# Kernel optimization log

Hardware: AMD Instinct MI355X
Metric: run time of the kernel (lower is better)

## Reference

```python
import jax, jax.numpy as jnp
import numpy as np

K = 10  # hardcoded in the module
F = 3 + 3 * K + 3 * K + K + 3  # 76-dim per-point feature


def setup_inputs() -> dict:
    key = jax.random.key(0)
    k0, k1, k2, k3, k4 = jax.random.split(key, 5)
    B, N = 4, 8192
    input_cloud = jax.random.normal(k0, (B, N, 3), dtype=jnp.float32)
    # Single shared MLP (76 -> 64 -> 3); the original instantiates a fresh
    # randomly-initialized MLP per point, which a fused kernel replaces with
    # shared weights.
    W1 = jax.random.normal(k1, (F, 64), dtype=jnp.float32) * 0.1
    b1 = jax.random.normal(k2, (64,), dtype=jnp.float32) * 0.01
    W2 = jax.random.normal(k3, (64, 3), dtype=jnp.float32) * 0.1
    b2 = jax.random.normal(k4, (3,), dtype=jnp.float32) * 0.01
    return {"input_cloud": input_cloud, "W1": W1, "b1": b1, "W2": W2, "b2": b2}


def _knn_indices(cloud):
    # squared pairwise distances (same ordering as cdist), topk smallest
    sq = jnp.sum(cloud * cloud, axis=-1)  # [B,N]
    d2 = sq[:, :, None] + sq[:, None, :] - 2.0 * jnp.einsum("bnd,bmd->bnm", cloud, cloud)
    _, idx = jax.lax.top_k(-d2, K + 1)  # [B,N,K+1], smallest first (self at 0)
    return idx[:, :, 1:]  # drop self -> [B,N,K]


def reference(input_cloud, W1, b1, W2, b2):
    B, N, _ = input_cloud.shape
    knn_idx = _knn_indices(input_cloud)  # [B,N,K] int32

    # gather neighbors: [B,N,K,3]
    neighbors = jnp.take_along_axis(input_cloud[:, None, :, :],
                                    knn_idx[:, :, :, None], axis=2)
    center = input_cloud  # [B,N,3]
    rel = neighbors - center[:, :, None, :]           # [B,N,K,3]
    dists = jnp.sqrt(jnp.sum(rel * rel, axis=-1))     # [B,N,K]

    # per-point 3x3 covariance of the K neighbors (unbiased, like torch.cov)
    mean = jnp.mean(neighbors, axis=2, keepdims=True)  # [B,N,1,3]
    cen = neighbors - mean
    cov = jnp.einsum("bnki,bnkj->bnij", cen, cen) / (K - 1)  # [B,N,3,3]

    eig = jnp.linalg.eigvalsh(cov)          # ascending [B,N,3]
    l1, l2, l3 = eig[..., 2], eig[..., 1], eig[..., 0]  # descending order
    linearity = (l1 - l2) / l1
    planarity = (l2 - l3) / l1
    scattering = l3 / l1
    geom = jnp.stack([linearity, planarity, scattering], axis=-1)  # [B,N,3]

    feats = jnp.concatenate(
        [center,
         neighbors.reshape(B, N, 3 * K),
         rel.reshape(B, N, 3 * K),
         dists,
         geom], axis=-1)  # [B,N,76]

    h = jax.nn.relu(jnp.einsum("bnf,fh->bnh", feats, W1) + b1)
    out = jax.nn.relu(jnp.einsum("bnh,ho->bno", h, W2) + b2)  # [B,N,3]
    return out
```

## Files before the change

### kernel.cpp

```cpp
#include <hip/hip_runtime.h>
#include <math.h>

#define KNN    10
#define NPTS   8192
#define HID    64
#define NF     76
#define Q      16
#define CAP    64
#define F32_INF __uint_as_float(0x7F800000u)

typedef float v2f __attribute__((ext_vector_type(2)));

__device__ __forceinline__ float rl(float v, int lane) {
    return __int_as_float(__builtin_amdgcn_readlane(__float_as_int(v), lane));
}

__global__ __launch_bounds__(256) void soa_kernel(const float* __restrict__ cloud,
                                                  float* __restrict__ soa) {
    const int i = blockIdx.x * 256 + threadIdx.x;
    const float x = cloud[i * 3 + 0];
    const float y = cloud[i * 3 + 1];
    const float z = cloud[i * 3 + 2];
    soa[i]             = x;
    soa[4 * NPTS + i]  = y;
    soa[8 * NPTS + i]  = z;
}

__global__ __launch_bounds__(512) void knn_kernel(const float* __restrict__ soa,
                                                  unsigned short* __restrict__ knn_idx) {
    __shared__ unsigned long long coll[CAP][33];
    __shared__ float pk[8][Q][17];
    __shared__ float tau_s[32];
    __shared__ int   cnt[32];

    const int t    = threadIdx.x;
    const int w    = t >> 6;
    const int lane = t & 63;
    const int g    = w >> 2;
    const int h    = w & 3;
    const int bx   = blockIdx.x;
    const int b    = bx >> 8;
    const int n_base = (bx & 255) * 32 + g * Q;
    const int lq_base = g * Q;
    const int cb0 = h * (NPTS / 4);

    const float* __restrict__ xs = soa + (size_t)b * NPTS;
    const float* __restrict__ ys = xs + 4 * NPTS;
    const float* __restrict__ zs = xs + 8 * NPTS;

    if (t < 32) cnt[t] = 0;

    v2f qx_p[8], qy_p[8], qz_p[8];
    {
        const int ql = n_base + (lane & 15);
        const float lx = xs[ql];
        const float ly = ys[ql];
        const float lz = zs[ql];
#pragma unroll
        for (int j = 0; j < 8; ++j) {
            qx_p[j] = (v2f){ rl(lx, 2 * j), rl(lx, 2 * j + 1) };
            qy_p[j] = (v2f){ rl(ly, 2 * j), rl(ly, 2 * j + 1) };
            qz_p[j] = (v2f){ rl(lz, 2 * j), rl(lz, 2 * j + 1) };
        }
    }

    v2f vmin2[8];
#pragma unroll
    for (int j = 0; j < 8; ++j) vmin2[j] = (v2f){ F32_INF, F32_INF };

    {
        float cx0 = xs[cb0 + lane];
        float cy0 = ys[cb0 + lane];
        float cz0 = zs[cb0 + lane];
        for (int ti = 0; ti < NPTS / 4 / 64; ++ti) {
            const int c1 = cb0 + (((ti + 1) & 31) * 64) + lane;
            const float nx0 = xs[c1];
            const float ny0 = ys[c1];
            const float nz0 = zs[c1];
            const float aw  = fmaf(cz0, cz0, fmaf(cy0, cy0, cx0 * cx0));
            const v2f aw2  = (v2f){ aw, aw };
            const v2f a2x2 = (v2f){ -2.0f * cx0, -2.0f * cx0 };
            const v2f a2y2 = (v2f){ -2.0f * cy0, -2.0f * cy0 };
            const v2f a2z2 = (v2f){ -2.0f * cz0, -2.0f * cz0 };
#pragma unroll
            for (int j = 0; j < 8; ++j) {
                const v2f v = __builtin_elementwise_fma(a2x2, qx_p[j],
                              __builtin_elementwise_fma(a2y2, qy_p[j],
                              __builtin_elementwise_fma(a2z2, qz_p[j], aw2)));
                vmin2[j] = __builtin_elementwise_min(vmin2[j], v);
            }
            cx0 = nx0; cy0 = ny0; cz0 = nz0;
        }
    }

#pragma unroll
    for (int qq = 0; qq < Q; ++qq) {
        float v = vmin2[qq >> 1][qq & 1];
        v = fminf(v, __shfl_xor(v, 32, 64));
        v = fminf(v, __shfl_xor(v, 16, 64));
        if (lane < 16) pk[w][qq][lane] = v;
    }
    __syncthreads();

    if (h == 0) {
        float md[KNN + 1];
#pragma unroll
        for (int s = 0; s <= KNN; ++s) md[s] = F32_INF;
        const int qsel = lane & 15;
#pragma unroll
        for (int cc = 0; cc < 64; ++cc) {
            float d = pk[g * 4 + (cc >> 4)][qsel][cc & 15];
#pragma unroll
            for (int u = 0; u <= KNN; ++u) {
                const float lo = fminf(md[u], d);
                d = fmaxf(md[u], d);
                md[u] = lo;
            }
        }
        if (lane < 16) tau_s[lq_base + lane] = md[KNN] + 1e-3f;
    }
    __syncthreads();

    float taum[Q];
    {
        const float tv = tau_s[lq_base + (lane & 15)];
#pragma unroll
        for (int qq = 0; qq < Q; ++qq) taum[qq] = rl(tv, qq);
    }

    {
        float cx2 = xs[cb0 + lane];
        float cy2 = ys[cb0 + lane];
        float cz2 = zs[cb0 + lane];
        int jcur = cb0 + lane;
        for (int ti = 0; ti < NPTS / 4 / 64; ++ti) {
            const int c1 = cb0 + (((ti + 1) & 31) * 64) + lane;
            const float nx2 = xs[c1];
            const float ny2 = ys[c1];
            const float nz2 = zs[c1];
            const float aw  = fmaf(cz2, cz2, fmaf(cy2, cy2, cx2 * cx2));
            const v2f aw2  = (v2f){ aw, aw };
            const v2f a2x2 = (v2f){ -2.0f * cx2, -2.0f * cx2 };
            const v2f a2y2 = (v2f){ -2.0f * cy2, -2.0f * cy2 };
            const v2f a2z2 = (v2f){ -2.0f * cz2, -2.0f * cz2 };
#pragma unroll
            for (int j = 0; j < 8; ++j) {
                const v2f v = __builtin_elementwise_fma(a2x2, qx_p[j],
                              __builtin_elementwise_fma(a2y2, qy_p[j],
                              __builtin_elementwise_fma(a2z2, qz_p[j], aw2)));
#pragma unroll
                for (int half = 0; half < 2; ++half) {
                    const int qq = 2 * j + half;
                    if (__builtin_expect(v[half] <= taum[qq], 0)) {
                        const float qx = qx_p[j][half];
                        const float qy = qy_p[j][half];
                        const float qz = qz_p[j][half];
                        const float qs = fmaf(qz, qz, fmaf(qy, qy, qx * qx));
                        const float dot = fmaf(cz2, qz, fmaf(cy2, qy, cx2 * qx));
                        const float d2 = fmaf(-2.0f, dot, qs + aw);
                        const unsigned int fb = __float_as_uint(d2);
                        const unsigned int m =
                            fb ^ ((unsigned int)((int)fb >> 31) | 0x80000000u);
                        const unsigned long long key =
                            ((unsigned long long)m << 13) | (unsigned long long)(unsigned)jcur;
                        const int slot = atomicAdd(&cnt[lq_base + qq], 1);
                        if (slot < CAP) coll[slot][lq_base + qq] = key;
                    }
                }
            }
            cx2 = nx2; cy2 = ny2; cz2 = nz2;
            jcur += 64;
        }
    }
    __syncthreads();

    if (t < 32) {
        const int m = cnt[t];
        int mc = m;
#pragma unroll
        for (int off = 1; off < 32; off <<= 1)
            mc = max(mc, __shfl_xor(mc, off, 64));
        mc = __builtin_amdgcn_readfirstlane(mc);

        const int n = (bx & 255) * 32 + t;

        unsigned long long md[KNN + 1];
#pragma unroll
        for (int s = 0; s <= KNN; ++s) md[s] = ~0ULL;

        if (mc <= CAP) {
            for (int cc = 0; cc < mc; ++cc) {
                unsigned long long key = (cc < m) ? coll[cc][t] : ~0ULL;
#pragma unroll
                for (int u = 0; u <= KNN; ++u) {
                    const bool lt = key < md[u];
                    const unsigned long long lo = lt ? key : md[u];
                    key = lt ? md[u] : key;
                    md[u] = lo;
                }
            }
        } else {
            const float qx = xs[n];
            const float qy = ys[n];
            const float qz = zs[n];
            const float qs = fmaf(qz, qz, fmaf(qy, qy, qx * qx));
            for (int j = 0; j < NPTS; ++j) {
                const float px = xs[j];
                const float py = ys[j];
                const float pz = zs[j];
                const float pw = fmaf(pz, pz, fmaf(py, py, px * px));
                const float dot = fmaf(pz, qz, fmaf(py, qy, px * qx));
                const float d2 = fmaf(-2.0f, dot, qs + pw);
                const unsigned int fb = __float_as_uint(d2);
                const unsigned int mm =
                    fb ^ ((unsigned int)((int)fb >> 31) | 0x80000000u);
                unsigned long long key =
                    ((unsigned long long)mm << 13) | (unsigned long long)j;
                key = (j == n) ? ~0ULL : key;
#pragma unroll
                for (int u = 0; u <= KNN; ++u) {
                    const bool lt = key < md[u];
                    const unsigned long long lo = lt ? key : md[u];
                    key = lt ? md[u] : key;
                    md[u] = lo;
                }
            }
        }

        unsigned short* outp = knn_idx + ((size_t)b * NPTS + n) * KNN;
        int outc = 0;
#pragma unroll
        for (int u = 0; u <= KNN; ++u) {
            const int idx = (int)(md[u] & 8191u);
            if (outc < KNN && idx != n) outp[outc++] = (unsigned short)idx;
        }
    }
}

__global__ __launch_bounds__(256) void feat_mlp_kernel(const float* __restrict__ cloud,
                                                       const float* __restrict__ W1,
                                                       const float* __restrict__ b1,
                                                       const float* __restrict__ W2,
                                                       const float* __restrict__ b2,
                                                       const unsigned short* __restrict__ knn_idx,
                                                       float* __restrict__ out) {
    __shared__ float w1s[NF * 68];
    __shared__ float b1s[HID];
    __shared__ float w2s[HID * 3];
    __shared__ float b2s[3];
    __shared__ float fs[64][NF + 1];

    const int t = threadIdx.x;
    for (int idx = t; idx < NF * HID; idx += 256)
        w1s[(idx >> 6) * 68 + (idx & 63)] = W1[idx];
    if (t < HID) b1s[t] = b1[t];
    if (t < HID * 3) w2s[t] = W2[t];
    if (t < 3) b2s[t] = b2[t];

    const int pl   = t >> 2;
    const int s    = t & 3;
    const int subh = t & 1;
    const int subf = (t >> 1) & 1;
    const int gid = blockIdx.x * 64 + pl;
    const int b = gid >> 13;
    const int n = gid & (NPTS - 1);
    const float* cb = cloud + (size_t)b * NPTS * 3;

    {
        const float cx = cb[n * 3 + 0];
        const float cy = cb[n * 3 + 1];
        const float cz = cb[n * 3 + 2];

        const int kbase = (s == 0) ? 0 : (s == 1) ? 3 : (s == 2) ? 6 : 8;
        const int kcnt  = (s < 2) ? 3 : 2;

        float nx[3], ny[3], nz[3];
        const unsigned short* ki = knn_idx + (size_t)gid * KNN;
        for (int kk = 0; kk < kcnt; ++kk) {
            const int j = ki[kbase + kk];
            nx[kk] = cb[j * 3 + 0];
            ny[kk] = cb[j * 3 + 1];
            nz[kk] = cb[j * 3 + 2];
        }

        float* fr = fs[pl];
        if (s == 0) { fr[0] = cx; fr[1] = cy; fr[2] = cz; }
        for (int kk = 0; kk < kcnt; ++kk) {
            const int k = kbase + kk;
            fr[3 + 3 * k + 0] = nx[kk];
            fr[3 + 3 * k + 1] = ny[kk];
            fr[3 + 3 * k + 2] = nz[kk];
            const float rx = nx[kk] - cx, ry = ny[kk] - cy, rz = nz[kk] - cz;
            fr[33 + 3 * k + 0] = rx;
            fr[33 + 3 * k + 1] = ry;
            fr[33 + 3 * k + 2] = rz;
            fr[63 + k] = sqrtf(fmaf(rz, rz, fmaf(ry, ry, rx * rx)));
        }

        float smx = 0.f, smy = 0.f, smz = 0.f;
        for (int kk = 0; kk < kcnt; ++kk) { smx += nx[kk]; smy += ny[kk]; smz += nz[kk]; }
#define QSUM(v) { v += __shfl_xor(v, 1, 64); v += __shfl_xor(v, 2, 64); }
        QSUM(smx); QSUM(smy); QSUM(smz);
        const float mx = smx * (1.0f / KNN);
        const float my = smy * (1.0f / KNN);
        const float mz = smz * (1.0f / KNN);

        float c00 = 0.f, c01 = 0.f, c02 = 0.f, c11 = 0.f, c12 = 0.f, c22 = 0.f;
        for (int kk = 0; kk < kcnt; ++kk) {
            const float ex = nx[kk] - mx, ey = ny[kk] - my, ez = nz[kk] - mz;
            c00 = fmaf(ex, ex, c00); c01 = fmaf(ex, ey, c01); c02 = fmaf(ex, ez, c02);
            c11 = fmaf(ey, ey, c11); c12 = fmaf(ey, ez, c12); c22 = fmaf(ez, ez, c22);
        }
        QSUM(c00); QSUM(c01); QSUM(c02); QSUM(c11); QSUM(c12); QSUM(c22);
#undef QSUM
        const float sc = 1.0f / (KNN - 1);
        c00 *= sc; c01 *= sc; c02 *= sc; c11 *= sc; c12 *= sc; c22 *= sc;

        const float qd = (c00 + c11 + c22) * (1.0f / 3.0f);
        const float pp1 = c01 * c01 + c02 * c02 + c12 * c12;
        const float d00 = c00 - qd, d11 = c11 - qd, d22 = c22 - qd;
        const float p2 = d00 * d00 + d11 * d11 + d22 * d22 + 2.0f * pp1;
        float l1, l2, l3;
        if (p2 < 1e-30f) {
            l1 = l2 = l3 = qd;
        } else {
            const float p = sqrtf(p2 * (1.0f / 6.0f));
            const float inv = 1.0f / p;
            const float e00 = d00 * inv, e11 = d11 * inv, e22 = d22 * inv;
            const float e01 = c01 * inv, e02 = c02 * inv, e12 = c12 * inv;
            float detB = e00 * (e11 * e22 - e12 * e12)
                       - e01 * (e01 * e22 - e12 * e02)
                       + e02 * (e01 * e12 - e11 * e02);
            float r = 0.5f * detB;
            r = fminf(1.0f, fmaxf(-1.0f, r));
            const float phi = acosf(r) * (1.0f / 3.0f);
            l1 = qd + 2.0f * p * __cosf(phi);
            l3 = qd + 2.0f * p * __cosf(phi + 2.0943951023931953f);
            l2 = 3.0f * qd - l1 - l3;
        }
        if (s == 0) {
            fr[73] = (l1 - l2) / l1;
            fr[74] = (l2 - l3) / l1;
            fr[75] = l3 / l1;
        }
    }

    __syncthreads();

    const float* fr = fs[pl];
    const int f0 = subf * 38;

    float h[32];
#pragma unroll
    for (int j = 0; j < 32; ++j) h[j] = (subf == 0) ? b1s[subh * 32 + j] : 0.0f;

#pragma unroll 2
    for (int ff = 0; ff < 38; ++ff) {
        const int f = f0 + ff;
        const float v = fr[f];
        const float4* w4 = reinterpret_cast<const float4*>(w1s + f * 68 + subh * 32);
#pragma unroll
        for (int j4 = 0; j4 < 8; ++j4) {
            const float4 w = w4[j4];
            h[4 * j4 + 0] = fmaf(v, w.x, h[4 * j4 + 0]);
            h[4 * j4 + 1] = fmaf(v, w.y, h[4 * j4 + 1]);
            h[4 * j4 + 2] = fmaf(v, w.z, h[4 * j4 + 2]);
            h[4 * j4 + 3] = fmaf(v, w.w, h[4 * j4 + 3]);
        }
    }

#pragma unroll
    for (int j = 0; j < 32; ++j) h[j] += __shfl_xor(h[j], 2, 64);

    float o0 = 0.f, o1 = 0.f, o2 = 0.f;
#pragma unroll
    for (int j = 0; j < 32; ++j) {
        const float r = fmaxf(h[j], 0.0f);
        const int jj = subh * 32 + j;
        o0 = fmaf(r, w2s[jj * 3 + 0], o0);
        o1 = fmaf(r, w2s[jj * 3 + 1], o1);
        o2 = fmaf(r, w2s[jj * 3 + 2], o2);
    }
    o0 += __shfl_xor(o0, 1, 64);
    o1 += __shfl_xor(o1, 1, 64);
    o2 += __shfl_xor(o2, 1, 64);

    if ((t & 3) == 0) {
        float* op = out + (size_t)gid * 3;
        op[0] = fmaxf(o0 + b2s[0], 0.0f);
        op[1] = fmaxf(o1 + b2s[1], 0.0f);
        op[2] = fmaxf(o2 + b2s[2], 0.0f);
    }
}

extern "C" void kernel_launch(void* const* d_in, const int* in_sizes, int n_in,
                              void* d_out, int out_size, void* d_ws, size_t ws_size,
                              hipStream_t stream) {
    const float* cloud = (const float*)d_in[0];
    const float* W1    = (const float*)d_in[1];
    const float* b1    = (const float*)d_in[2];
    const float* W2    = (const float*)d_in[3];
    const float* b2    = (const float*)d_in[4];
    float* out = (float*)d_out;

    unsigned short* knn = (unsigned short*)d_ws;
    float* soa = (float*)((char*)d_ws + 655360);

    soa_kernel<<<dim3(128), dim3(256), 0, stream>>>(cloud, soa);
    knn_kernel<<<dim3(1024), dim3(512), 0, stream>>>(soa, knn);
    feat_mlp_kernel<<<dim3(512), dim3(256), 0, stream>>>(cloud, W1, b1, W2, b2, knn, out);
}
```

Before: 170.6 us.

## Stage candidate points through double-buffered shared memory in KNN scans

Both candidate-scan passes of the KNN kernel now load 256 candidate coordinates per step cooperatively into a double-buffered LDS tile, with each wave reading its 64-point slice from shared memory. Previously each wave streamed its own quarter of the cloud directly from global memory. The goal is to coalesce global loads and share them across the two query groups in a block, which halves redundant global traffic. The cost is a __syncthreads per tile, 32 per pass, and it also changes the order in which candidates are visited.

```diff
diff --git a/kernel.cpp b/kernel.cpp
--- a/kernel.cpp
+++ b/kernel.cpp
@@ -32,6 +32,7 @@
     __shared__ float pk[8][Q][17];
     __shared__ float tau_s[32];
     __shared__ int   cnt[32];
+    __shared__ float stg[2][3][256];
 
     const int t    = threadIdx.x;
     const int w    = t >> 6;
@@ -42,7 +43,9 @@
     const int b    = bx >> 8;
     const int n_base = (bx & 255) * 32 + g * Q;
     const int lq_base = g * Q;
-    const int cb0 = h * (NPTS / 4);
+    const int h64  = h * 64;
+    const int tl   = t & 255;
+    const bool loA = (w < 4);
 
     const float* __restrict__ xs = soa + (size_t)b * NPTS;
     const float* __restrict__ ys = xs + 4 * NPTS;
@@ -64,19 +67,26 @@
         }
     }
 
+    if (loA) { stg[0][0][tl] = xs[tl]; stg[0][2][tl] = zs[tl]; }
+    else     { stg[0][1][tl] = ys[tl]; }
+    __syncthreads();
+
     v2f vmin2[8];
 #pragma unroll
     for (int j = 0; j < 8; ++j) vmin2[j] = (v2f){ F32_INF, F32_INF };
 
     {
-        float cx0 = xs[cb0 + lane];
-        float cy0 = ys[cb0 + lane];
-        float cz0 = zs[cb0 + lane];
-        for (int ti = 0; ti < NPTS / 4 / 64; ++ti) {
-            const int c1 = cb0 + (((ti + 1) & 31) * 64) + lane;
-            const float nx0 = xs[c1];
-            const float ny0 = ys[c1];
-            const float nz0 = zs[c1];
+        int cur = 0;
+        for (int k = 0; k < 32; ++k) {
+            const int kn = ((k + 1) & 31) * 256;
+            float s0 = 0.0f, s1 = 0.0f;
+            if (loA) { s0 = xs[kn + tl]; s1 = zs[kn + tl]; }
+            else     { s0 = ys[kn + tl]; }
+
+            const int ci = h64 + lane;
+            const float cx0 = stg[cur][0][ci];
+            const float cy0 = stg[cur][1][ci];
+            const float cz0 = stg[cur][2][ci];
             const float aw  = fmaf(cz0, cz0, fmaf(cy0, cy0, cx0 * cx0));
             const v2f aw2  = (v2f){ aw, aw };
             const v2f a2x2 = (v2f){ -2.0f * cx0, -2.0f * cx0 };
@@ -89,7 +99,12 @@
                               __builtin_elementwise_fma(a2z2, qz_p[j], aw2)));
                 vmin2[j] = __builtin_elementwise_min(vmin2[j], v);
             }
-            cx0 = nx0; cy0 = ny0; cz0 = nz0;
+
+            const int nb = cur ^ 1;
+            if (loA) { stg[nb][0][tl] = s0; stg[nb][2][tl] = s1; }
+            else     { stg[nb][1][tl] = s0; }
+            __syncthreads();
+            cur = nb;
         }
     }
 
@@ -128,16 +143,23 @@
         for (int qq = 0; qq < Q; ++qq) taum[qq] = rl(tv, qq);
     }
 
+    if (loA) { stg[0][0][tl] = xs[tl]; stg[0][2][tl] = zs[tl]; }
+    else     { stg[0][1][tl] = ys[tl]; }
+    __syncthreads();
+
     {
-        float cx2 = xs[cb0 + lane];
-        float cy2 = ys[cb0 + lane];
-        float cz2 = zs[cb0 + lane];
-        int jcur = cb0 + lane;
-        for (int ti = 0; ti < NPTS / 4 / 64; ++ti) {
-            const int c1 = cb0 + (((ti + 1) & 31) * 64) + lane;
-            const float nx2 = xs[c1];
-            const float ny2 = ys[c1];
-            const float nz2 = zs[c1];
+        int cur = 0;
+        for (int k = 0; k < 32; ++k) {
+            const int kn = ((k + 1) & 31) * 256;
+            float s0 = 0.0f, s1 = 0.0f;
+            if (loA) { s0 = xs[kn + tl]; s1 = zs[kn + tl]; }
+            else     { s0 = ys[kn + tl]; }
+
+            const int ci = h64 + lane;
+            const float cx2 = stg[cur][0][ci];
+            const float cy2 = stg[cur][1][ci];
+            const float cz2 = stg[cur][2][ci];
+            const int jcur  = k * 256 + ci;
             const float aw  = fmaf(cz2, cz2, fmaf(cy2, cy2, cx2 * cx2));
             const v2f aw2  = (v2f){ aw, aw };
             const v2f a2x2 = (v2f){ -2.0f * cx2, -2.0f * cx2 };
@@ -168,8 +190,12 @@
                     }
                 }
             }
-            cx2 = nx2; cy2 = ny2; cz2 = nz2;
-            jcur += 64;
+
+            const int nb = cur ^ 1;
+            if (loA) { stg[nb][0][tl] = s0; stg[nb][2][tl] = s1; }
+            else     { stg[nb][1][tl] = s0; }
+            __syncthreads();
+            cur = nb;
         }
     }
     __syncthreads();
```

Result: slower. 193.5 us (+13.5%).
